# Performance work log

Hardware: AMD Instinct MI355X
Metric: run time of the kernel (lower is better)

Reference implementation:

```python
import jax, jax.numpy as jnp
import numpy as np

N = 50000
E = 800000
IN_F = 128
OUT_F = 128


def setup_inputs() -> dict:
    key = jax.random.key(0)
    k1, k2, k3, k4, k5 = jax.random.split(key, 5)
    x = jax.random.normal(k1, (N, IN_F), dtype=jnp.float32)
    # sparse adjacency as COO edge list: row = dst (aggregating node), col = src
    edge_index = jax.random.randint(k2, (2, E), 0, N, dtype=jnp.int64)
    edge_weight = jax.random.uniform(k3, (E,), dtype=jnp.float32)
    # nn.Linear(in_features, out_features): W is [out, in], b is [out]
    W = jax.random.normal(k4, (OUT_F, IN_F), dtype=jnp.float32) * (1.0 / np.sqrt(IN_F))
    b = jax.random.normal(k5, (OUT_F,), dtype=jnp.float32) * 0.01
    return {"x": x, "edge_index": edge_index, "edge_weight": edge_weight, "W": W, "b": b}


def reference(x, edge_index, edge_weight, W, b):
    # hidden = self.linear(x)  -> [N, out]
    hidden = jnp.einsum("ni,oi->no", x, W) + b
    # out = adj @ hidden (SpMM): out[dst] += w_e * hidden[src]
    dst = edge_index[0]
    src = edge_index[1]
    msgs = edge_weight[:, None] * hidden[src]  # [E, out]
    out = jax.ops.segment_sum(msgs, dst, num_segments=x.shape[0])
    return out
```

## Files before the change

### kernel.cpp

```cpp
#include <hip/hip_runtime.h>
#include <hip/hip_bf16.h>

#define N_NODES 50000
#define N_EDGES 800000
#define FEAT    128
#define N_TILES (N_NODES / 16)
#define MAXD    32
#define OVF_CAP 16384
#define NODES_PER_GRP 6250
#define CHUNK   2048
#define NCHUNK  ((N_EDGES + CHUNK - 1) / CHUNK)

using short8  = __attribute__((ext_vector_type(8))) short;
using float4v = __attribute__((ext_vector_type(4))) float;


__device__ __forceinline__ unsigned short f2b(float f) {
    __hip_bfloat16 h = __float2bfloat16(f);
    return __builtin_bit_cast(unsigned short, h);
}

__global__ void k_init(const int* __restrict__ ei, int* __restrict__ flag,
                       int* __restrict__ fill) {
    int i = blockIdx.x * blockDim.x + threadIdx.x;
    if (i < N_NODES) fill[i] = 0;
    if (blockIdx.x == 0 && threadIdx.x < 64) {
        unsigned long long m = __ballot(ei[2 * threadIdx.x + 1] != 0);
        if (threadIdx.x == 0) { flag[0] = (m == 0ULL) ? 1 : 0; flag[1] = 0; }
    }
}

__global__ __launch_bounds__(256) void k_gemm(const float* __restrict__ x,
                                              const float* __restrict__ W,
                                              const float* __restrict__ bias,
                                              unsigned short* __restrict__ hidden) {
    __shared__ __align__(16) unsigned short Wlds[128 * 136];
    const int t = threadIdx.x;
    for (int j = 0; j < 16; ++j) {
        int idx4 = j * 256 + t;
        float4v wv = *(const float4v*)(W + (size_t)idx4 * 4);
        int r = (idx4 * 4) >> 7;
        int c = (idx4 * 4) & 127;
        unsigned short* p = &Wlds[r * 136 + c];
        p[0] = f2b(wv[0]); p[1] = f2b(wv[1]); p[2] = f2b(wv[2]); p[3] = f2b(wv[3]);
    }
    __syncthreads();

    const int wave = t >> 6;
    const int lane = t & 63;
    int tile = blockIdx.x * 4 + wave;
    if (tile >= N_TILES) tile = N_TILES - 1;
    const int rowBase = tile * 16;
    const int m    = lane & 15;
    const int quad = lane >> 4;

    float4v acc[8];
    for (int i = 0; i < 8; ++i) acc[i] = (float4v){0.f, 0.f, 0.f, 0.f};

    for (int kk = 0; kk < 4; ++kk) {
        const int k0 = kk * 32 + quad * 8;
        const float* ap = x + (size_t)(rowBase + m) * FEAT + k0;
        float4v a0 = *(const float4v*)(ap);
        float4v a1 = *(const float4v*)(ap + 4);
        short8 af;
        for (int j = 0; j < 4; ++j) { af[j] = (short)f2b(a0[j]); af[4 + j] = (short)f2b(a1[j]); }
        for (int nt = 0; nt < 8; ++nt) {
            short8 bf = *(const short8*)&Wlds[(nt * 16 + m) * 136 + k0];
            acc[nt] = __builtin_amdgcn_mfma_f32_16x16x32_bf16(af, bf, acc[nt], 0, 0, 0);
        }
    }

    const int r0 = rowBase + quad * 4;
    for (int nt = 0; nt < 8; ++nt) {
        const int col = nt * 16 + m;
        const float bc = bias[col];
        for (int r = 0; r < 4; ++r) {
            hidden[(size_t)(r0 + r) * FEAT + col] = f2b(acc[nt][r] + bc);
        }
    }
}

__global__ __launch_bounds__(256) void k_scatter(const int* __restrict__ ei,
                                                 const float* __restrict__ wt,
                                                 const int* __restrict__ flag,
                                                 int* __restrict__ fill,
                                                 unsigned int* __restrict__ slots,
                                                 int2* __restrict__ ovf) {
    const int grp = blockIdx.x & 7;
    const int lo  = grp * NODES_PER_GRP;
    const int hi  = lo + NODES_PER_GRP;
    const int sh  = flag[0];
    const int e0  = (blockIdx.x >> 3) * CHUNK + threadIdx.x;

    #pragma unroll
    for (int i = 0; i < CHUNK / 256; ++i) {
        int e = e0 + i * 256;
        if (e >= N_EDGES) break;
        int dst = ei[(size_t)e << sh];
        if ((unsigned)dst >= N_NODES) dst = 0;
        if (dst < lo || dst >= hi) continue;
        int src = ei[(size_t)(N_EDGES + e) << sh];
        if ((unsigned)src >= N_NODES) src = 0;
        unsigned int rec = ((unsigned int)f2b(wt[e]) << 16) | (unsigned int)src;
        int pos = atomicAdd(&fill[dst], 1);
        if (pos < MAXD) {
            slots[(size_t)dst * MAXD + pos] = rec;
        } else {
            int op = atomicAdd((int*)&((int*)flag)[1], 1);
            if (op < OVF_CAP) { int2 r; r.x = dst; r.y = (int)rec; ovf[op] = r; }
        }
    }
}

__global__ __launch_bounds__(256) void k_agg(const int* __restrict__ fill,
                                             const unsigned int* __restrict__ slots,
                                             const unsigned int* __restrict__ hid,
                                             const int* __restrict__ flag,
                                             const int2* __restrict__ ovf,
                                             float* __restrict__ out) {
    const int wave = threadIdx.x >> 6;
    const int lane = threadIdx.x & 63;
    const int node = blockIdx.x * 4 + wave;
    const int grp  = lane >> 4;
    const int sub  = lane & 15;

    const int degf = fill[node];
    const int deg  = (degf > MAXD) ? MAXD : degf;
    const unsigned int* sl = slots + (size_t)node * MAXD;

    float acc[8];
    #pragma unroll
    for (int j = 0; j < 8; ++j) acc[j] = 0.f;

    float    ws[8];
    unsigned srcs[8];
    #pragma unroll
    for (int it = 0; it < 8; ++it) {
        const int e = it * 4;
        uint4 recs = *(const uint4*)(sl + e);
        unsigned rec = (grp < 2) ? (grp == 0 ? recs.x : recs.y)
                                 : (grp == 2 ? recs.z : recs.w);
        const bool v = (e + grp) < deg;
        ws[it]   = v ? __uint_as_float(rec & 0xffff0000u) : 0.f;
        srcs[it] = v ? (rec & 0xffffu) : 0u;
    }

    #pragma unroll
    for (int it = 0; it < 8; ++it) {
        uint4 h = *((const uint4*)(hid + (size_t)srcs[it] * 64) + sub);
        const float w = ws[it];
        acc[0] = fmaf(w, __uint_as_float((h.x & 0xffffu) << 16), acc[0]);
        acc[1] = fmaf(w, __uint_as_float(h.x & 0xffff0000u),     acc[1]);
        acc[2] = fmaf(w, __uint_as_float((h.y & 0xffffu) << 16), acc[2]);
        acc[3] = fmaf(w, __uint_as_float(h.y & 0xffff0000u),     acc[3]);
        acc[4] = fmaf(w, __uint_as_float((h.z & 0xffffu) << 16), acc[4]);
        acc[5] = fmaf(w, __uint_as_float(h.z & 0xffff0000u),     acc[5]);
        acc[6] = fmaf(w, __uint_as_float((h.w & 0xffffu) << 16), acc[6]);
        acc[7] = fmaf(w, __uint_as_float(h.w & 0xffff0000u),     acc[7]);
    }

    if (degf > MAXD) {
        int n = flag[1]; if (n > OVF_CAP) n = OVF_CAP;
        for (int i = 0; i < n; ++i) {
            int2 r = ovf[i];
            if (r.x != node || (i & 3) != grp) continue;
            unsigned rec = (unsigned)r.y;
            float w = __uint_as_float(rec & 0xffff0000u);
            unsigned src = rec & 0xffffu;
            uint4 h = *((const uint4*)(hid + (size_t)src * 64) + sub);
            acc[0] = fmaf(w, __uint_as_float((h.x & 0xffffu) << 16), acc[0]);
            acc[1] = fmaf(w, __uint_as_float(h.x & 0xffff0000u),     acc[1]);
            acc[2] = fmaf(w, __uint_as_float((h.y & 0xffffu) << 16), acc[2]);
            acc[3] = fmaf(w, __uint_as_float(h.y & 0xffff0000u),     acc[3]);
            acc[4] = fmaf(w, __uint_as_float((h.z & 0xffffu) << 16), acc[4]);
            acc[5] = fmaf(w, __uint_as_float(h.z & 0xffff0000u),     acc[5]);
            acc[6] = fmaf(w, __uint_as_float((h.w & 0xffffu) << 16), acc[6]);
            acc[7] = fmaf(w, __uint_as_float(h.w & 0xffff0000u),     acc[7]);
        }
    }

    #pragma unroll
    for (int j = 0; j < 8; ++j) {
        float a = acc[j];
        a += __shfl_xor(a, 16, 64);
        a += __shfl_xor(a, 32, 64);
        acc[j] = a;
    }

    if (lane < 16) {
        float* o = out + (size_t)node * FEAT + sub * 8;
        *(float4*)(o)     = make_float4(acc[0], acc[1], acc[2], acc[3]);
        *(float4*)(o + 4) = make_float4(acc[4], acc[5], acc[6], acc[7]);
    }
}

extern "C" void kernel_launch(void* const* d_in, const int* in_sizes, int n_in,
                              void* d_out, int out_size, void* d_ws, size_t ws_size,
                              hipStream_t stream) {
    const float* x  = (const float*)d_in[0];
    const int*   ei = (const int*)d_in[1];
    const float* ew = (const float*)d_in[2];
    const float* W  = (const float*)d_in[3];
    const float* b  = (const float*)d_in[4];
    float* out = (float*)d_out;

    int*  flag = (int*)d_ws;
    int*  fill = flag + 16;
    int2* ovf  = (int2*)(fill + 50048);
    unsigned int* slots = (unsigned int*)(ovf + OVF_CAP);
    unsigned short* hidden = (unsigned short*)(slots + (size_t)N_NODES * MAXD);

    k_init   <<<(N_NODES + 255) / 256, 256, 0, stream>>>(ei, flag, fill);
    k_gemm   <<<(N_TILES + 3) / 4, 256, 0, stream>>>(x, W, b, hidden);
    k_scatter<<<NCHUNK * 8, 256, 0, stream>>>(ei, ew, flag, fill, slots, ovf);
    k_agg    <<<N_NODES / 4, 256, 0, stream>>>(fill, slots, (const unsigned int*)hidden,
                                               flag, ovf, out);
}
```

Baseline: 187.0 us.

## Split hidden into feature quarters and aggregate in four cache-resident passes

The GEMM now writes hidden in four column-quarter planes of 32 bf16 features each, 3.2MB per plane. The aggregation runs as four launches, one per quarter, so each pass's random gathers hit a smaller working set that fits in cache better. Each wave now handles 16 nodes with 4 lanes per node, using a loop bounded by the max degree in the wave and shuffles to share edge records. The scatter loads become nontemporal. The cost is rereading slots and fill four times plus extra launch overhead.

```diff
diff --git a/kernel.cpp b/kernel.cpp
--- a/kernel.cpp
+++ b/kernel.cpp
@@ -10,6 +10,8 @@
 #define NODES_PER_GRP 6250
 #define CHUNK   2048
 #define NCHUNK  ((N_EDGES + CHUNK - 1) / CHUNK)
+#define QTR_ELEMS ((size_t)N_NODES * 32)
+#define AGG_BLOCKS ((N_NODES + 63) / 64)
 
 using short8  = __attribute__((ext_vector_type(8))) short;
 using float4v = __attribute__((ext_vector_type(4))) float;
@@ -74,8 +76,9 @@
     for (int nt = 0; nt < 8; ++nt) {
         const int col = nt * 16 + m;
         const float bc = bias[col];
+        unsigned short* hq = hidden + (size_t)(col >> 5) * QTR_ELEMS + (col & 31);
         for (int r = 0; r < 4; ++r) {
-            hidden[(size_t)(r0 + r) * FEAT + col] = f2b(acc[nt][r] + bc);
+            hq[(size_t)(r0 + r) * 32] = f2b(acc[nt][r] + bc);
         }
     }
 }
@@ -96,12 +99,13 @@
     for (int i = 0; i < CHUNK / 256; ++i) {
         int e = e0 + i * 256;
         if (e >= N_EDGES) break;
-        int dst = ei[(size_t)e << sh];
+        int dst = __builtin_nontemporal_load(ei + ((size_t)e << sh));
         if ((unsigned)dst >= N_NODES) dst = 0;
         if (dst < lo || dst >= hi) continue;
-        int src = ei[(size_t)(N_EDGES + e) << sh];
+        int src = __builtin_nontemporal_load(ei + ((size_t)(N_EDGES + e) << sh));
         if ((unsigned)src >= N_NODES) src = 0;
-        unsigned int rec = ((unsigned int)f2b(wt[e]) << 16) | (unsigned int)src;
+        float w = __builtin_nontemporal_load(wt + e);
+        unsigned int rec = ((unsigned int)f2b(w) << 16) | (unsigned int)src;
         int pos = atomicAdd(&fill[dst], 1);
         if (pos < MAXD) {
             slots[(size_t)dst * MAXD + pos] = rec;
@@ -112,43 +116,49 @@
     }
 }
 
-__global__ __launch_bounds__(256) void k_agg(const int* __restrict__ fill,
-                                             const unsigned int* __restrict__ slots,
-                                             const unsigned int* __restrict__ hid,
-                                             const int* __restrict__ flag,
-                                             const int2* __restrict__ ovf,
-                                             float* __restrict__ out) {
+__global__ __launch_bounds__(256) void k_aggq(const int* __restrict__ fill,
+                                              const unsigned int* __restrict__ slots,
+                                              const unsigned short* __restrict__ hq,
+                                              const int* __restrict__ flag,
+                                              const int2* __restrict__ ovf,
+                                              float* __restrict__ out,
+                                              int qpass) {
+    const int lane = threadIdx.x & 63;
     const int wave = threadIdx.x >> 6;
-    const int lane = threadIdx.x & 63;
-    const int node = blockIdx.x * 4 + wave;
-    const int grp  = lane >> 4;
-    const int sub  = lane & 15;
-
-    const int degf = fill[node];
+    const int wid  = blockIdx.x * 4 + wave;
+    const int g    = lane >> 2;
+    const int sub  = lane & 3;
+    const int node = wid * 16 + g;
+    const bool alive = node < N_NODES;
+    const int nc = alive ? node : 0;
+
+    const int degf = fill[nc];
     const int deg  = (degf > MAXD) ? MAXD : degf;
-    const unsigned int* sl = slots + (size_t)node * MAXD;
+
+    unsigned recv[8];
+    const unsigned* sl = slots + (size_t)nc * MAXD;
+    #pragma unroll
+    for (int k = 0; k < 8; ++k) recv[k] = sl[sub + 4 * k];
+
+    int md = deg;
+    md = max(md, __shfl_xor(md, 4, 64));
+    md = max(md, __shfl_xor(md, 8, 64));
+    md = max(md, __shfl_xor(md, 16, 64));
+    md = max(md, __shfl_xor(md, 32, 64));
+
+    const uint4* hq4 = (const uint4*)hq;
+    const int base_lane = lane & 0xFC;
 
     float acc[8];
     #pragma unroll
     for (int j = 0; j < 8; ++j) acc[j] = 0.f;
 
-    float    ws[8];
-    unsigned srcs[8];
-    #pragma unroll
-    for (int it = 0; it < 8; ++it) {
-        const int e = it * 4;
-        uint4 recs = *(const uint4*)(sl + e);
-        unsigned rec = (grp < 2) ? (grp == 0 ? recs.x : recs.y)
-                                 : (grp == 2 ? recs.z : recs.w);
-        const bool v = (e + grp) < deg;
-        ws[it]   = v ? __uint_as_float(rec & 0xffff0000u) : 0.f;
-        srcs[it] = v ? (rec & 0xffffu) : 0u;
-    }
-
-    #pragma unroll
-    for (int it = 0; it < 8; ++it) {
-        uint4 h = *((const uint4*)(hid + (size_t)srcs[it] * 64) + sub);
-        const float w = ws[it];
+    for (int e = 0; e < md; ++e) {
+        unsigned rec = __shfl(recv[e >> 2], base_lane | (e & 3), 64);
+        const bool v = alive && (e < deg);
+        const float w = v ? __uint_as_float(rec & 0xffff0000u) : 0.f;
+        const unsigned src = v ? (rec & 0xffffu) : 0u;
+        uint4 h = hq4[(size_t)src * 4 + sub];
         acc[0] = fmaf(w, __uint_as_float((h.x & 0xffffu) << 16), acc[0]);
         acc[1] = fmaf(w, __uint_as_float(h.x & 0xffff0000u),     acc[1]);
         acc[2] = fmaf(w, __uint_as_float((h.y & 0xffffu) << 16), acc[2]);
@@ -163,11 +173,11 @@
         int n = flag[1]; if (n > OVF_CAP) n = OVF_CAP;
         for (int i = 0; i < n; ++i) {
             int2 r = ovf[i];
-            if (r.x != node || (i & 3) != grp) continue;
+            if (r.x != node) continue;
             unsigned rec = (unsigned)r.y;
             float w = __uint_as_float(rec & 0xffff0000u);
             unsigned src = rec & 0xffffu;
-            uint4 h = *((const uint4*)(hid + (size_t)src * 64) + sub);
+            uint4 h = hq4[(size_t)src * 4 + sub];
             acc[0] = fmaf(w, __uint_as_float((h.x & 0xffffu) << 16), acc[0]);
             acc[1] = fmaf(w, __uint_as_float(h.x & 0xffff0000u),     acc[1]);
             acc[2] = fmaf(w, __uint_as_float((h.y & 0xffffu) << 16), acc[2]);
@@ -179,16 +189,8 @@
         }
     }
 
-    #pragma unroll
-    for (int j = 0; j < 8; ++j) {
-        float a = acc[j];
-        a += __shfl_xor(a, 16, 64);
-        a += __shfl_xor(a, 32, 64);
-        acc[j] = a;
-    }
-
-    if (lane < 16) {
-        float* o = out + (size_t)node * FEAT + sub * 8;
+    if (alive) {
+        float* o = out + (size_t)node * FEAT + qpass * 32 + sub * 8;
         *(float4*)(o)     = make_float4(acc[0], acc[1], acc[2], acc[3]);
         *(float4*)(o + 4) = make_float4(acc[4], acc[5], acc[6], acc[7]);
     }
@@ -213,6 +215,8 @@
     k_init   <<<(N_NODES + 255) / 256, 256, 0, stream>>>(ei, flag, fill);
     k_gemm   <<<(N_TILES + 3) / 4, 256, 0, stream>>>(x, W, b, hidden);
     k_scatter<<<NCHUNK * 8, 256, 0, stream>>>(ei, ew, flag, fill, slots, ovf);
-    k_agg    <<<N_NODES / 4, 256, 0, stream>>>(fill, slots, (const unsigned int*)hidden,
-                                               flag, ovf, out);
-}
+    for (int q = 0; q < 4; ++q) {
+        k_aggq<<<AGG_BLOCKS, 256, 0, stream>>>(fill, slots, hidden + (size_t)q * QTR_ELEMS,
+                                               flag, ovf, out, q);
+    }
+}
```

After: 199.7 us. 1.07x slower.
